# Kernel tuning notes

Measured on AMD Instinct MI355X. Metric: run time of the kernel, lower is better.

The kernel has to match this reference:

```python
import jax, jax.numpy as jnp
import numpy as np

L = 4
ND, ED, HD, NH = 128, 64, 256, 8
DH = HD // NH
NNODES = [40000, 10000, 2000, 400]
NEDGES = [320000, 160000, 32000, 6400]
LN_EPS = 1e-5


def setup_inputs() -> dict:
    key = jax.random.key(0)
    it = iter(jax.random.split(key, 40))
    d = {}
    for i in range(L):
        d[f"nodes{i}"] = jax.random.normal(next(it), (NNODES[i], ND), jnp.float32)
        d[f"edges{i}"] = jax.random.normal(next(it), (NEDGES[i], ED), jnp.float32)
        d[f"edge_index{i}"] = jax.random.randint(next(it), (2, NEDGES[i]), 0, NNODES[i])

    def lin(k, fin, fout):
        # Linear weight, fan-in scaled, stacked over L levels
        return jax.random.normal(k, (L, fin, fout), jnp.float32) / np.float32(np.sqrt(fin))

    d["Wq"] = lin(next(it), ND, HD); d["bq"] = jnp.zeros((L, HD), jnp.float32)
    d["Wk"] = lin(next(it), ND, HD); d["bk"] = jnp.zeros((L, HD), jnp.float32)
    d["Wv"] = lin(next(it), ND, HD); d["bv"] = jnp.zeros((L, HD), jnp.float32)
    d["We"] = lin(next(it), ED, NH); d["be"] = jnp.zeros((L, NH), jnp.float32)
    d["Wo"] = lin(next(it), HD, ND); d["bo"] = jnp.zeros((L, ND), jnp.float32)
    d["gamma"] = jnp.ones((L, ND), jnp.float32)
    d["beta"] = jnp.zeros((L, ND), jnp.float32)
    return d


def _attention_level(nodes, edges, ei, Wq, bq, Wk, bk, Wv, bv, We, be, Wo, bo, gamma, beta):
    n = nodes.shape[0]
    q = (nodes @ Wq + bq).reshape(n, NH, DH)
    k = (nodes @ Wk + bk).reshape(n, NH, DH)
    v = (nodes @ Wv + bv).reshape(n, NH, DH)
    edge_att = edges @ We + be                               # [E, NH]
    src, tgt = ei[0], ei[1]
    # per-edge multi-head dot-product scores with edge bias
    scores = jnp.einsum('ehd,ehd->eh', q[src], k[tgt]) / np.float32(np.sqrt(DH)) + edge_att
    # segment softmax over incoming edges of each target node (stable)
    m = jax.ops.segment_max(scores, tgt, num_segments=n)    # [N, NH]
    ex = jnp.exp(scores - m[tgt])
    denom = jax.ops.segment_sum(ex, tgt, num_segments=n)
    w = ex / denom[tgt]                                      # [E, NH]
    # weighted scatter-add aggregation
    agg = jax.ops.segment_sum(w[..., None] * v[tgt], tgt, num_segments=n).reshape(n, HD)
    x = nodes + (agg @ Wo + bo)                              # residual (dropout=identity in eval)
    mu = jnp.mean(x, axis=-1, keepdims=True)
    var = jnp.mean((x - mu) ** 2, axis=-1, keepdims=True)
    return gamma * (x - mu) / jnp.sqrt(var + LN_EPS) + beta


def reference(nodes0, edges0, edge_index0, nodes1, edges1, edge_index1,
              nodes2, edges2, edge_index2, nodes3, edges3, edge_index3,
              Wq, bq, Wk, bk, Wv, bv, We, be, Wo, bo, gamma, beta):
    graphs = [(nodes0, edges0, edge_index0), (nodes1, edges1, edge_index1),
              (nodes2, edges2, edge_index2), (nodes3, edges3, edge_index3)]
    outs = []
    for i, (nd, eg, ei) in enumerate(graphs):
        outs.append(_attention_level(nd, eg, ei, Wq[i], bq[i], Wk[i], bk[i],
                                     Wv[i], bv[i], We[i], be[i], Wo[i], bo[i],
                                     gamma[i], beta[i]))
    return tuple(outs)
```

## Files before the change

kernel.cpp:

```cpp
#include <hip/hip_runtime.h>


#define N0 40000
#define N1 10000
#define N2 2000
#define N3 400
#define NTOT 52400
#define E0 320000
#define E1 160000
#define E2 32000
#define E3 6400

#define WS_WCB_OFF 65536
#define WS_CC_OFF  196608

typedef __bf16 bf16x8 __attribute__((ext_vector_type(8)));
typedef __bf16 bf16x4 __attribute__((ext_vector_type(4)));
typedef float  f32x4  __attribute__((ext_vector_type(4)));

#define XS 136
#define YS 133

__global__ void hgc_flags(const int* __restrict__ e0, const int* __restrict__ e1,
                          const int* __restrict__ e2, const int* __restrict__ e3,
                          unsigned char* __restrict__ flags)
{
    const int tid = threadIdx.x;
    const int b = blockIdx.x;
    const int* ei; int e, E, off;
    if (b < 1250)      { ei = e0; e = b * 256 + tid;          E = E0; off = 0; }
    else if (b < 1875) { ei = e1; e = (b - 1250) * 256 + tid; E = E1; off = N0; }
    else if (b < 2000) { ei = e2; e = (b - 1875) * 256 + tid; E = E2; off = N0 + N1; }
    else               { ei = e3; e = (b - 2000) * 256 + tid; E = E3; off = N0 + N1 + N2; }
    int tgt = ei[E + e];
    flags[off + tgt] = (unsigned char)1;
}

__global__ __launch_bounds__(128)
void hgc_wct(const float* __restrict__ Wv, const float* __restrict__ bv,
             const float* __restrict__ Wo, const float* __restrict__ bo,
             __bf16* __restrict__ WcB, float* __restrict__ cc)
{
    __shared__ float sv[256];
    const int b = blockIdx.x, j = threadIdx.x;
    const bool is_cc = (b >= 512);
    const int l = is_cc ? (b - 512) : (b >> 7);
    const int k = is_cc ? 0 : (b & 127);
    const float* src = is_cc ? (bv + l * 256) : (Wv + ((size_t)l * 128 + k) * 256);
    sv[j] = src[j]; sv[j + 128] = src[j + 128];
    __syncthreads();
    const float* wo = Wo + (size_t)l * 256 * 128 + j;
    float a0 = 0.f, a1 = 0.f, a2 = 0.f, a3 = 0.f;
#pragma unroll 4
    for (int t = 0; t < 256; t += 4) {
        a0 += sv[t + 0] * wo[(t + 0) * 128];
        a1 += sv[t + 1] * wo[(t + 1) * 128];
        a2 += sv[t + 2] * wo[(t + 2) * 128];
        a3 += sv[t + 3] * wo[(t + 3) * 128];
    }
    float r = (a0 + a1) + (a2 + a3);
    if (is_cc) cc[l * 128 + j] = r + bo[l * 128 + j];
    else       WcB[((size_t)l * 128 + j) * 128 + k] = (__bf16)r;
}

__global__ __launch_bounds__(256, 3)
void hgc_main(const float* __restrict__ n0, const float* __restrict__ n1,
              const float* __restrict__ n2, const float* __restrict__ n3,
              const unsigned char* __restrict__ flags,
              const __bf16* __restrict__ WcB, const float* __restrict__ cc,
              const float* __restrict__ bo, const float* __restrict__ gamma,
              const float* __restrict__ beta, float* __restrict__ out)
{
    __shared__ __align__(16) char smem[17408 + 34816];
    __shared__ float s_mean[64];
    __shared__ float s_rstd[64];
    __bf16* sX = (__bf16*)smem;
    __bf16* sW = (__bf16*)(smem + 17408);
    float*  sY = (float*)smem;

    const int tid = threadIdx.x;
    const int b = blockIdx.x;
    int l, lb, Nl, goff; const float* nd;
    if (b < 625)      { l = 0; lb = b;       Nl = N0; goff = 0;     nd = n0; }
    else if (b < 782) { l = 1; lb = b - 625; Nl = N1; goff = 40000; nd = n1; }
    else if (b < 814) { l = 2; lb = b - 782; Nl = N2; goff = 50000; nd = n2; }
    else              { l = 3; lb = b - 814; Nl = N3; goff = 52000; nd = n3; }
    const int rbase = lb * 64;

#pragma unroll
    for (int i = 0; i < 8; ++i) {
        int f = tid + 256 * i;
        int r = f >> 5, c4 = f & 31;
        int rr = rbase + r; if (rr >= Nl) rr = Nl - 1;
        float4 v = ((const float4*)(nd + (size_t)rr * 128))[c4];
        bf16x4 p = { (__bf16)v.x, (__bf16)v.y, (__bf16)v.z, (__bf16)v.w };
        *(bf16x4*)(sX + r * XS + c4 * 4) = p;
    }
    const __bf16* wsl = WcB + (size_t)l * 16384;
#pragma unroll
    for (int i = 0; i < 8; ++i) {
        int g = tid + 256 * i;
        int r = g >> 4, o = g & 15;
        *(bf16x8*)(sW + r * XS + o * 8) = *(const bf16x8*)(wsl + r * 128 + o * 8);
    }
    __syncthreads();

    const int m = tid & 15;
    const int q = (tid >> 4) & 3;
    const int w = tid >> 6;
    const __bf16* ax = sX + (w * 16 + m) * XS + q * 8;
    const __bf16* bx = sW + m * XS + q * 8;

    f32x4 acc[8] = {};
#pragma unroll
    for (int ks = 0; ks < 4; ++ks) {
        bf16x8 a = *(const bf16x8*)(ax + ks * 32);
#pragma unroll
        for (int nt = 0; nt < 8; ++nt) {
            bf16x8 bfr = *(const bf16x8*)(bx + nt * 16 * XS + ks * 32);
            acc[nt] = __builtin_amdgcn_mfma_f32_16x16x32_bf16(a, bfr, acc[nt], 0, 0, 0);
        }
    }
    __syncthreads();

    {
        float* yb = sY + (w * 16 + q * 4) * YS + m;
#pragma unroll
        for (int nt = 0; nt < 8; ++nt)
#pragma unroll
            for (int rg = 0; rg < 4; ++rg)
                yb[rg * YS + nt * 16] = acc[nt][rg];
    }
    __syncthreads();

    {
        const int r = tid >> 2, qt = tid & 3;
        int rr = rbase + r; int rc = (rr < Nl) ? rr : (Nl - 1);
        const float4* xrow = (const float4*)(nd + (size_t)rc * 128 + qt * 32);
        const int fl = flags[goff + rc];
        float* yr = sY + r * YS + qt * 32;
        const float* ccl = cc + l * 128 + qt * 32;
        const float* bol = bo + l * 128 + qt * 32;
        float sum = 0.f, sq = 0.f;
#pragma unroll
        for (int i = 0; i < 8; ++i) {
            float4 xv = xrow[i];
#pragma unroll
            for (int u = 0; u < 4; ++u) {
                int jj = i * 4 + u;
                float xc = (u == 0) ? xv.x : (u == 1) ? xv.y : (u == 2) ? xv.z : xv.w;
                float y = yr[jj];
                float t = fl ? (y + ccl[jj]) : bol[jj];
                float vv = xc + t;
                yr[jj] = vv;
                sum += vv; sq += vv * vv;
            }
        }
        sum += __shfl_xor(sum, 1); sq += __shfl_xor(sq, 1);
        sum += __shfl_xor(sum, 2); sq += __shfl_xor(sq, 2);
        if (qt == 0) {
            float mean = sum * (1.f / 128.f);
            float var  = sq * (1.f / 128.f) - mean * mean;
            s_mean[r] = mean;
            s_rstd[r] = rsqrtf(var + 1e-5f);
        }
    }
    __syncthreads();

    {
        const int c = tid & 127, h = tid >> 7;
        const float g  = gamma[l * 128 + c];
        const float bt = beta[l * 128 + c];
#pragma unroll 4
        for (int i = 0; i < 32; ++i) {
            int qrow = h + 2 * i;
            int rr = rbase + qrow;
            if (rr >= Nl) break;
            float v = sY[qrow * YS + c];
            out[((size_t)(goff + rr)) * 128 + c] = g * (v - s_mean[qrow]) * s_rstd[qrow] + bt;
        }
    }
}

extern "C" void kernel_launch(void* const* d_in, const int* in_sizes, int n_in,
                              void* d_out, int out_size, void* d_ws, size_t ws_size,
                              hipStream_t stream)
{
    const float* n0 = (const float*)d_in[0];
    const int*   e0 = (const int*)d_in[2];
    const float* n1 = (const float*)d_in[3];
    const int*   e1 = (const int*)d_in[5];
    const float* n2 = (const float*)d_in[6];
    const int*   e2 = (const int*)d_in[8];
    const float* n3 = (const float*)d_in[9];
    const int*   e3 = (const int*)d_in[11];
    const float* Wv    = (const float*)d_in[16];
    const float* bv    = (const float*)d_in[17];
    const float* Wo    = (const float*)d_in[20];
    const float* bo    = (const float*)d_in[21];
    const float* gamma = (const float*)d_in[22];
    const float* beta  = (const float*)d_in[23];

    unsigned char* flags = (unsigned char*)d_ws;
    __bf16* WcB = (__bf16*)((char*)d_ws + WS_WCB_OFF);
    float*  cc  = (float*)((char*)d_ws + WS_CC_OFF);

    hipMemsetAsync(flags, 0, NTOT, stream);
    hgc_flags<<<2025, 256, 0, stream>>>(e0, e1, e2, e3, flags);
    hgc_wct<<<516, 128, 0, stream>>>(Wv, bv, Wo, bo, WcB, cc);

    hgc_main<<<821, 256, 0, stream>>>(n0, n1, n2, n3, flags, WcB, cc,
                                      bo, gamma, beta, (float*)d_out);
}
```

Before: 228.4 us.

## Fuse prep kernels and keep node tile fp32 in LDS, epilogue from registers

Merges the flag-marking and weight-combining kernels into one launch, with int4 edge loads and two weight rows per block. In the main kernel the node tile stays in LDS as fp32 and is converted to bf16 at MFMA time. The B operand is read straight from global rather than staged in LDS. The residual and LayerNorm statistics are computed directly from the MFMA accumulators, which removes the shared-memory Y round trip, one barrier and the second global read of the node rows. It also raises occupancy to 4 and vectorises the output stores, at the cost of uncached global B loads per wave.

After: 223.2 us. 2.3% less time.

```diff
diff --git a/kernel.cpp b/kernel.cpp
--- a/kernel.cpp
+++ b/kernel.cpp
@@ -15,55 +15,71 @@
 #define WS_CC_OFF  196608
 
 typedef __bf16 bf16x8 __attribute__((ext_vector_type(8)));
-typedef __bf16 bf16x4 __attribute__((ext_vector_type(4)));
 typedef float  f32x4  __attribute__((ext_vector_type(4)));
 
-#define XS 136
-#define YS 133
-
-__global__ void hgc_flags(const int* __restrict__ e0, const int* __restrict__ e1,
-                          const int* __restrict__ e2, const int* __restrict__ e3,
-                          unsigned char* __restrict__ flags)
+#define XS 132
+
+__global__ __launch_bounds__(256)
+void hgc_prep(const int* __restrict__ e0, const int* __restrict__ e1,
+              const int* __restrict__ e2, const int* __restrict__ e3,
+              const float* __restrict__ Wv, const float* __restrict__ bv,
+              const float* __restrict__ Wo, const float* __restrict__ bo,
+              unsigned char* __restrict__ flags, __bf16* __restrict__ WcB,
+              float* __restrict__ cc)
 {
-    const int tid = threadIdx.x;
-    const int b = blockIdx.x;
-    const int* ei; int e, E, off;
-    if (b < 1250)      { ei = e0; e = b * 256 + tid;          E = E0; off = 0; }
-    else if (b < 1875) { ei = e1; e = (b - 1250) * 256 + tid; E = E1; off = N0; }
-    else if (b < 2000) { ei = e2; e = (b - 1875) * 256 + tid; E = E2; off = N0 + N1; }
-    else               { ei = e3; e = (b - 2000) * 256 + tid; E = E3; off = N0 + N1 + N2; }
-    int tgt = ei[E + e];
-    flags[off + tgt] = (unsigned char)1;
+    __shared__ float sv[512];
+    const int b = blockIdx.x, tid = threadIdx.x;
+    if (b < 509) {
+        const int* ei; int E, off, lb;
+        if (b < 313)      { ei = e0; E = E0; off = 0;            lb = b; }
+        else if (b < 470) { ei = e1; E = E1; off = N0;           lb = b - 313; }
+        else if (b < 502) { ei = e2; E = E2; off = N0 + N1;      lb = b - 470; }
+        else              { ei = e3; E = E3; off = N0 + N1 + N2; lb = b - 502; }
+        int e = lb * 1024 + tid * 4;
+        if (e < E) {
+            int4 t4 = *(const int4*)(ei + E + e);
+            flags[off + t4.x] = 1; flags[off + t4.y] = 1;
+            flags[off + t4.z] = 1; flags[off + t4.w] = 1;
+        }
+        return;
+    }
+    if (b < 765) {
+        const int w = b - 509, l = w >> 6, kp = w & 63;
+        const float* src = Wv + ((size_t)l * 128 + kp * 2) * 256;
+        sv[tid] = src[tid]; sv[tid + 256] = src[tid + 256];
+        __syncthreads();
+        const int half = tid >> 7, j = tid & 127;
+        const float* svh = sv + half * 256;
+        const float* wo = Wo + (size_t)l * 256 * 128 + j;
+        float a0 = 0.f, a1 = 0.f, a2 = 0.f, a3 = 0.f;
+#pragma unroll 4
+        for (int t = 0; t < 256; t += 4) {
+            a0 += svh[t + 0] * wo[(t + 0) * 128];
+            a1 += svh[t + 1] * wo[(t + 1) * 128];
+            a2 += svh[t + 2] * wo[(t + 2) * 128];
+            a3 += svh[t + 3] * wo[(t + 3) * 128];
+        }
+        WcB[((size_t)l * 128 + j) * 128 + kp * 2 + half] = (__bf16)((a0 + a1) + (a2 + a3));
+        return;
+    }
+    {
+        const int idx = (b - 765) * 256 + tid;
+        const int l = idx >> 7, j = idx & 127;
+        const float* wo = Wo + (size_t)l * 256 * 128 + j;
+        const float* bvl = bv + l * 256;
+        float a0 = 0.f, a1 = 0.f, a2 = 0.f, a3 = 0.f;
+#pragma unroll 4
+        for (int t = 0; t < 256; t += 4) {
+            a0 += bvl[t + 0] * wo[(t + 0) * 128];
+            a1 += bvl[t + 1] * wo[(t + 1) * 128];
+            a2 += bvl[t + 2] * wo[(t + 2) * 128];
+            a3 += bvl[t + 3] * wo[(t + 3) * 128];
+        }
+        cc[idx] = (a0 + a1) + (a2 + a3) + bo[idx];
+    }
 }
 
-__global__ __launch_bounds__(128)
-void hgc_wct(const float* __restrict__ Wv, const float* __restrict__ bv,
-             const float* __restrict__ Wo, const float* __restrict__ bo,
-             __bf16* __restrict__ WcB, float* __restrict__ cc)
-{
-    __shared__ float sv[256];
-    const int b = blockIdx.x, j = threadIdx.x;
-    const bool is_cc = (b >= 512);
-    const int l = is_cc ? (b - 512) : (b >> 7);
-    const int k = is_cc ? 0 : (b & 127);
-    const float* src = is_cc ? (bv + l * 256) : (Wv + ((size_t)l * 128 + k) * 256);
-    sv[j] = src[j]; sv[j + 128] = src[j + 128];
-    __syncthreads();
-    const float* wo = Wo + (size_t)l * 256 * 128 + j;
-    float a0 = 0.f, a1 = 0.f, a2 = 0.f, a3 = 0.f;
-#pragma unroll 4
-    for (int t = 0; t < 256; t += 4) {
-        a0 += sv[t + 0] * wo[(t + 0) * 128];
-        a1 += sv[t + 1] * wo[(t + 1) * 128];
-        a2 += sv[t + 2] * wo[(t + 2) * 128];
-        a3 += sv[t + 3] * wo[(t + 3) * 128];
-    }
-    float r = (a0 + a1) + (a2 + a3);
-    if (is_cc) cc[l * 128 + j] = r + bo[l * 128 + j];
-    else       WcB[((size_t)l * 128 + j) * 128 + k] = (__bf16)r;
-}
-
-__global__ __launch_bounds__(256, 3)
+__global__ __launch_bounds__(256, 4)
 void hgc_main(const float* __restrict__ n0, const float* __restrict__ n1,
               const float* __restrict__ n2, const float* __restrict__ n3,
               const unsigned char* __restrict__ flags,
@@ -71,12 +87,9 @@
               const float* __restrict__ bo, const float* __restrict__ gamma,
               const float* __restrict__ beta, float* __restrict__ out)
 {
-    __shared__ __align__(16) char smem[17408 + 34816];
+    __shared__ float sX[64 * XS];
     __shared__ float s_mean[64];
     __shared__ float s_rstd[64];
-    __bf16* sX = (__bf16*)smem;
-    __bf16* sW = (__bf16*)(smem + 17408);
-    float*  sY = (float*)smem;
 
     const int tid = threadIdx.x;
     const int b = blockIdx.x;
@@ -93,91 +106,92 @@
         int r = f >> 5, c4 = f & 31;
         int rr = rbase + r; if (rr >= Nl) rr = Nl - 1;
         float4 v = ((const float4*)(nd + (size_t)rr * 128))[c4];
-        bf16x4 p = { (__bf16)v.x, (__bf16)v.y, (__bf16)v.z, (__bf16)v.w };
-        *(bf16x4*)(sX + r * XS + c4 * 4) = p;
-    }
-    const __bf16* wsl = WcB + (size_t)l * 16384;
-#pragma unroll
-    for (int i = 0; i < 8; ++i) {
-        int g = tid + 256 * i;
-        int r = g >> 4, o = g & 15;
-        *(bf16x8*)(sW + r * XS + o * 8) = *(const bf16x8*)(wsl + r * 128 + o * 8);
+        *(float4*)(sX + r * XS + c4 * 4) = v;
     }
     __syncthreads();
 
     const int m = tid & 15;
     const int q = (tid >> 4) & 3;
     const int w = tid >> 6;
-    const __bf16* ax = sX + (w * 16 + m) * XS + q * 8;
-    const __bf16* bx = sW + m * XS + q * 8;
+    const float* axf = sX + (w * 16 + m) * XS + q * 8;
+    const __bf16* wl = WcB + (size_t)l * 16384 + (size_t)m * 128 + q * 8;
 
     f32x4 acc[8] = {};
 #pragma unroll
     for (int ks = 0; ks < 4; ++ks) {
-        bf16x8 a = *(const bf16x8*)(ax + ks * 32);
+        float4 xa = *(const float4*)(axf + ks * 32);
+        float4 xb = *(const float4*)(axf + ks * 32 + 4);
+        bf16x8 a = { (__bf16)xa.x, (__bf16)xa.y, (__bf16)xa.z, (__bf16)xa.w,
+                     (__bf16)xb.x, (__bf16)xb.y, (__bf16)xb.z, (__bf16)xb.w };
 #pragma unroll
         for (int nt = 0; nt < 8; ++nt) {
-            bf16x8 bfr = *(const bf16x8*)(bx + nt * 16 * XS + ks * 32);
+            bf16x8 bfr = *(const bf16x8*)(wl + nt * 2048 + ks * 32);
             acc[nt] = __builtin_amdgcn_mfma_f32_16x16x32_bf16(a, bfr, acc[nt], 0, 0, 0);
         }
     }
+
+    {
+        const int r0 = w * 16 + q * 4;
+        int fl[4];
+#pragma unroll
+        for (int rg = 0; rg < 4; ++rg) {
+            int rr = rbase + r0 + rg; if (rr >= Nl) rr = Nl - 1;
+            fl[rg] = flags[goff + rr];
+        }
+        float cc8[8], bo8[8];
+#pragma unroll
+        for (int nt = 0; nt < 8; ++nt) {
+            cc8[nt] = cc[l * 128 + m + 16 * nt];
+            bo8[nt] = bo[l * 128 + m + 16 * nt];
+        }
+        float sum[4] = {}, sq[4] = {};
+#pragma unroll
+        for (int rg = 0; rg < 4; ++rg) {
+            float* xr = sX + (r0 + rg) * XS + m;
+#pragma unroll
+            for (int nt = 0; nt < 8; ++nt) {
+                float x = xr[16 * nt];
+                float t = fl[rg] ? (acc[nt][rg] + cc8[nt]) : bo8[nt];
+                float v = x + t;
+                xr[16 * nt] = v;
+                sum[rg] += v; sq[rg] += v * v;
+            }
+        }
+#pragma unroll
+        for (int s = 1; s < 16; s <<= 1) {
+#pragma unroll
+            for (int rg = 0; rg < 4; ++rg) {
+                sum[rg] += __shfl_xor(sum[rg], s);
+                sq[rg]  += __shfl_xor(sq[rg], s);
+            }
+        }
+        if (m == 0) {
+#pragma unroll
+            for (int rg = 0; rg < 4; ++rg) {
+                float mean = sum[rg] * (1.f / 128.f);
+                float var  = sq[rg] * (1.f / 128.f) - mean * mean;
+                s_mean[r0 + rg] = mean;
+                s_rstd[r0 + rg] = rsqrtf(var + 1e-5f);
+            }
+        }
+    }
     __syncthreads();
 
     {
-        float* yb = sY + (w * 16 + q * 4) * YS + m;
-#pragma unroll
-        for (int nt = 0; nt < 8; ++nt)
-#pragma unroll
-            for (int rg = 0; rg < 4; ++rg)
-                yb[rg * YS + nt * 16] = acc[nt][rg];
-    }
-    __syncthreads();
-
-    {
-        const int r = tid >> 2, qt = tid & 3;
-        int rr = rbase + r; int rc = (rr < Nl) ? rr : (Nl - 1);
-        const float4* xrow = (const float4*)(nd + (size_t)rc * 128 + qt * 32);
-        const int fl = flags[goff + rc];
-        float* yr = sY + r * YS + qt * 32;
-        const float* ccl = cc + l * 128 + qt * 32;
-        const float* bol = bo + l * 128 + qt * 32;
-        float sum = 0.f, sq = 0.f;
-#pragma unroll
-        for (int i = 0; i < 8; ++i) {
-            float4 xv = xrow[i];
-#pragma unroll
-            for (int u = 0; u < 4; ++u) {
-                int jj = i * 4 + u;
-                float xc = (u == 0) ? xv.x : (u == 1) ? xv.y : (u == 2) ? xv.z : xv.w;
-                float y = yr[jj];
-                float t = fl ? (y + ccl[jj]) : bol[jj];
-                float vv = xc + t;
-                yr[jj] = vv;
-                sum += vv; sq += vv * vv;
-            }
-        }
-        sum += __shfl_xor(sum, 1); sq += __shfl_xor(sq, 1);
-        sum += __shfl_xor(sum, 2); sq += __shfl_xor(sq, 2);
-        if (qt == 0) {
-            float mean = sum * (1.f / 128.f);
-            float var  = sq * (1.f / 128.f) - mean * mean;
-            s_mean[r] = mean;
-            s_rstd[r] = rsqrtf(var + 1e-5f);
-        }
-    }
-    __syncthreads();
-
-    {
-        const int c = tid & 127, h = tid >> 7;
-        const float g  = gamma[l * 128 + c];
-        const float bt = beta[l * 128 + c];
+        const int c = (tid & 63) * 2, h = tid >> 6;
+        const float g0 = gamma[l * 128 + c],     g1 = gamma[l * 128 + c + 1];
+        const float t0 = beta[l * 128 + c],      t1 = beta[l * 128 + c + 1];
 #pragma unroll 4
-        for (int i = 0; i < 32; ++i) {
-            int qrow = h + 2 * i;
+        for (int i = 0; i < 16; ++i) {
+            int qrow = h + 4 * i;
             int rr = rbase + qrow;
-            if (rr >= Nl) break;
-            float v = sY[qrow * YS + c];
-            out[((size_t)(goff + rr)) * 128 + c] = g * (v - s_mean[qrow]) * s_rstd[qrow] + bt;
+            if (rr >= Nl) continue;
+            float2 v = *(const float2*)(sX + qrow * XS + c);
+            float mu = s_mean[qrow], rs = s_rstd[qrow];
+            float2 o;
+            o.x = g0 * (v.x - mu) * rs + t0;
+            o.y = g1 * (v.y - mu) * rs + t1;
+            *(float2*)(out + (size_t)(goff + rr) * 128 + c) = o;
         }
     }
 }
@@ -206,9 +220,8 @@
     float*  cc  = (float*)((char*)d_ws + WS_CC_OFF);
 
     hipMemsetAsync(flags, 0, NTOT, stream);
-    hgc_flags<<<2025, 256, 0, stream>>>(e0, e1, e2, e3, flags);
-    hgc_wct<<<516, 128, 0, stream>>>(Wv, bv, Wo, bo, WcB, cc);
-
+    hgc_prep<<<767, 256, 0, stream>>>(e0, e1, e2, e3, Wv, bv, Wo, bo,
+                                      flags, WcB, cc);
     hgc_main<<<821, 256, 0, stream>>>(n0, n1, n2, n3, flags, WcB, cc,
                                       bo, gamma, beta, (float*)d_out);
 }
```
